# Optimization experiments

Hardware: AMD Instinct MI355X
Metric: run time of the kernel (lower is better)

## Reference

```python
import jax, jax.numpy as jnp
import numpy as np

N_NODES = 50000   # num graph nodes
N_EDGES = 800000  # avg degree 16
D = 96            # in_channels == out_channels (residual aggr_out + x)


def setup_inputs() -> dict:
    key = jax.random.key(0)
    k0, k1, k2, k3, k4 = jax.random.split(key, 5)
    x = jax.random.normal(k0, (N_NODES, D), dtype=jnp.float32)
    edge_index = jax.random.randint(k1, (2, N_EDGES), 0, N_NODES)  # [2,E]: row0=src(j), row1=dst(i)
    edge_weight = jax.random.uniform(k2, (N_EDGES,), dtype=jnp.float32)
    pagerank = jax.random.uniform(k3, (N_NODES,), dtype=jnp.float32)
    # nn.Linear(in_channels, out_channels) params
    W = jax.random.normal(k4, (D, D), dtype=jnp.float32) / np.sqrt(D).astype(np.float32)
    b = jnp.zeros((D,), dtype=jnp.float32)
    return {"x": x, "edge_index": edge_index, "edge_weight": edge_weight,
            "pagerank": pagerank, "W": W, "b": b}


def reference(x, edge_index, edge_weight, pagerank, W, b):
    # CGCConv (PyG MessagePassing, aggr='add', flow source_to_target):
    #   message: edge_weight * x_j * pagerank_j   (gather from source nodes)
    #   aggregate: scatter-add to destination nodes
    #   update: Linear(aggr_out + x)
    src = edge_index[0]
    dst = edge_index[1]
    # [E, D] messages: per-edge gather-multiply
    msgs = edge_weight[:, None] * x[src] * pagerank[src][:, None]
    aggr = jax.ops.segment_sum(msgs, dst, num_segments=x.shape[0])  # [N, D]
    return (aggr + x) @ W.T + b
```

## Files before the change

kernel.cpp:

```cpp
#include <hip/hip_runtime.h>


constexpr int NN = 50000;
constexpr int NE = 800000;
constexpr int DD = 96;
constexpr int NB = 196;
constexpr int CAPB = 4608;
constexpr int EPB = 4096;
constexpr int NBLK = (NE + EPB - 1) / EPB;
constexpr int NCVT = (NN * DD / 4 + 511) / 512;

using s8v = __attribute__((ext_vector_type(8))) short;
using f4v = __attribute__((ext_vector_type(4))) float;

__device__ inline unsigned short f2bf(float f) {
    unsigned u = __float_as_uint(f);
    return (unsigned short)((u + 0x7FFFu + ((u >> 16) & 1u)) >> 16);
}
__device__ inline float bfh(unsigned short v) {
    return __uint_as_float((unsigned)v << 16);
}
__device__ inline unsigned long long pack_e(int meta, float c) {
    return (unsigned long long)(unsigned)meta |
           ((unsigned long long)(unsigned)__float_as_uint(c) << 32);
}

__global__ __launch_bounds__(256) void k_zero(int* __restrict__ cur1) {
    if (threadIdx.x < NB) cur1[threadIdx.x] = 0;
}

__global__ __launch_bounds__(512) void k_prep(const int* __restrict__ src,
                                              const int* __restrict__ dst,
                                              const float* __restrict__ ew,
                                              const float* __restrict__ pr,
                                              int* __restrict__ cur1,
                                              unsigned long long* __restrict__ stage,
                                              const float4* __restrict__ x4,
                                              ushort4* __restrict__ y16v) {
    int tid = threadIdx.x;
    if (blockIdx.x >= NBLK) {
        int i = (blockIdx.x - NBLK) * 512 + tid;
        if (i < NN * DD / 4) {
            float4 v = x4[i];
            y16v[i] = make_ushort4(f2bf(v.x), f2bf(v.y), f2bf(v.z), f2bf(v.w));
        }
        return;
    }
    __shared__ int h[256];
    __shared__ int gb[256];
    __shared__ int sc[256];
    __shared__ unsigned long long sorted[EPB];
    for (int i = tid; i < 256; i += 512) h[i] = 0;
    __syncthreads();
    int base = blockIdx.x * EPB;
    int n = min(EPB, NE - base);

    unsigned long long ent[8]; int bkt[8]; int lrk[8];
    #pragma unroll
    for (int j = 0; j < 8; j++) {
        int e = base + j * 512 + tid;
        bkt[j] = -1;
        if (e < NE) {
            int d = dst[e];
            int s = src[e];
            float c = ew[e] * pr[s];
            int bk = d >> 8;
            bkt[j] = bk;
            lrk[j] = atomicAdd(&h[bk], 1);
            ent[j] = pack_e(s | ((d & 255) << 16) | (bk << 24), c);
        }
    }
    __syncthreads();
    if (tid < 256) sc[tid] = h[tid];
    __syncthreads();
    #pragma unroll
    for (int o = 1; o < 256; o <<= 1) {
        int t = 0;
        if (tid < 256 && tid >= o) t = sc[tid - o];
        __syncthreads();
        if (tid < 256) sc[tid] += t;
        __syncthreads();
    }
    for (int i = tid; i < NB; i += 512)
        gb[i] = h[i] ? atomicAdd(&cur1[i], h[i]) : 0;
    __syncthreads();
    #pragma unroll
    for (int j = 0; j < 8; j++)
        if (bkt[j] >= 0)
            sorted[sc[bkt[j]] - h[bkt[j]] + lrk[j]] = ent[j];
    __syncthreads();
    for (int i = tid; i < n; i += 512) {
        unsigned long long e = sorted[i];
        int bk = ((int)(e >> 24)) & 0xff;
        stage[(size_t)bk * CAPB + gb[bk] + (i - (sc[bk] - h[bk]))] = e;
    }
}

__global__ __launch_bounds__(512) void k_sortB(unsigned long long* __restrict__ stage,
                                               const int* __restrict__ cur1,
                                               int* __restrict__ offs,
                                               int* __restrict__ counts) {
    __shared__ int h[256];
    __shared__ int sc[256];
    __shared__ unsigned sorted[CAPB];
    int b = blockIdx.x;
    int tid = threadIdx.x;
    size_t base = (size_t)b * CAPB;
    int n = cur1[b];

    for (int i = tid; i < 256; i += 512) h[i] = 0;
    __syncthreads();

    unsigned e32[9]; int dl[9]; int lrk[9];
    int m = 0;
    for (int i = tid; i < n; i += 512) {
        unsigned long long e = stage[base + i];
        int dloc = ((int)(e >> 16)) & 0xff;
        unsigned cb = (unsigned)(e >> 32);
        unsigned cbf = (cb + 0x7FFFu + ((cb >> 16) & 1u)) >> 16;
        e32[m] = ((unsigned)e & 0xffffu) | (cbf << 16);
        dl[m] = dloc;
        lrk[m] = atomicAdd(&h[dloc], 1);
        m++;
    }
    __syncthreads();
    if (tid < 256) sc[tid] = h[tid];
    __syncthreads();
    #pragma unroll
    for (int o = 1; o < 256; o <<= 1) {
        int t = 0;
        if (tid < 256 && tid >= o) t = sc[tid - o];
        __syncthreads();
        if (tid < 256) sc[tid] += t;
        __syncthreads();
    }
    m = 0;
    for (int i = tid; i < n; i += 512) {
        sorted[sc[dl[m]] - h[dl[m]] + lrk[m]] = e32[m];
        m++;
    }
    __syncthreads();
    unsigned* outp = (unsigned*)(stage + base);
    for (int i = tid; i < n; i += 512) outp[i] = sorted[i];
    if (tid < 256) {
        int d = (b << 8) + tid;
        if (d < NN) {
            offs[d] = (int)(2 * base) + sc[tid] - h[tid];
            counts[d] = h[tid];
        }
    }
}

__global__ __launch_bounds__(256) void k_pull(const ushort4* __restrict__ y16v,
                                              const float4* __restrict__ x4,
                                              const int* __restrict__ offs,
                                              const int* __restrict__ counts,
                                              const unsigned* __restrict__ ep,
                                              ushort4* __restrict__ io16v) {
    int g = blockIdx.x * 8 + (threadIdx.x >> 5);
    int lane = threadIdx.x & 31;
    if (g >= NN || lane >= 24) return;
    int beg = offs[g];
    int deg = counts[g];
    float ax = 0.f, ay = 0.f, az = 0.f, aw = 0.f;
    int k = 0;
    for (; k + 8 <= deg; k += 8) {
        unsigned e[8];
        #pragma unroll
        for (int j = 0; j < 8; j++) e[j] = ep[beg + k + j];
        ushort4 u[8];
        #pragma unroll
        for (int j = 0; j < 8; j++)
            u[j] = y16v[(size_t)(e[j] & 0xffff) * 24 + lane];
        #pragma unroll
        for (int j = 0; j < 8; j++) {
            float c = bfh((unsigned short)(e[j] >> 16));
            ax += c * bfh(u[j].x);
            ay += c * bfh(u[j].y);
            az += c * bfh(u[j].z);
            aw += c * bfh(u[j].w);
        }
    }
    for (; k + 4 <= deg; k += 4) {
        unsigned e[4];
        #pragma unroll
        for (int j = 0; j < 4; j++) e[j] = ep[beg + k + j];
        ushort4 u[4];
        #pragma unroll
        for (int j = 0; j < 4; j++)
            u[j] = y16v[(size_t)(e[j] & 0xffff) * 24 + lane];
        #pragma unroll
        for (int j = 0; j < 4; j++) {
            float c = bfh((unsigned short)(e[j] >> 16));
            ax += c * bfh(u[j].x);
            ay += c * bfh(u[j].y);
            az += c * bfh(u[j].z);
            aw += c * bfh(u[j].w);
        }
    }
    for (; k < deg; k++) {
        unsigned e = ep[beg + k];
        ushort4 u = y16v[(size_t)(e & 0xffff) * 24 + lane];
        float c = bfh((unsigned short)(e >> 16));
        ax += c * bfh(u.x);
        ay += c * bfh(u.y);
        az += c * bfh(u.z);
        aw += c * bfh(u.w);
    }
    float4 xn = x4[(size_t)g * 24 + lane];
    io16v[(size_t)g * 24 + lane] = make_ushort4(f2bf(ax + xn.x), f2bf(ay + xn.y),
                                                f2bf(az + xn.z), f2bf(aw + xn.w));
}

__global__ __launch_bounds__(256) void k_gemm(const unsigned short* __restrict__ io16,
                                              const float* __restrict__ W,
                                              const float* __restrict__ b,
                                              float* __restrict__ out) {
    __shared__ short bfr[18 * 64 * 8];
    int tid = threadIdx.x;
    for (int i = tid; i < 18 * 512; i += 256) {
        int f = i >> 9, r = i & 511;
        int lane = r >> 3, j = r & 7;
        int ks = f / 6, nt = f - 6 * ks;
        int n = nt * 16 + (lane & 15);
        int k = ks * 32 + (lane >> 4) * 8 + j;
        bfr[i] = (short)f2bf(W[n * DD + k]);
    }
    __syncthreads();

    int wave = tid >> 6, lane = tid & 63;
    int quad = lane >> 4, m16 = lane & 15;
    int r0 = blockIdx.x * 64 + wave * 16;
    int rowa = r0 + m16;
    if (rowa >= NN) rowa = NN - 1;

    f4v acc[6];
    #pragma unroll
    for (int nt = 0; nt < 6; nt++) acc[nt] = (f4v){0.f, 0.f, 0.f, 0.f};

    #pragma unroll
    for (int ks = 0; ks < 3; ks++) {
        s8v a = *(const s8v*)(io16 + (size_t)rowa * DD + ks * 32 + quad * 8);
        #pragma unroll
        for (int nt = 0; nt < 6; nt++) {
            s8v bb = *(const s8v*)&bfr[((ks * 6 + nt) * 64 + lane) * 8];
            acc[nt] = __builtin_amdgcn_mfma_f32_16x16x32_bf16(a, bb, acc[nt], 0, 0, 0);
        }
    }

    #pragma unroll
    for (int nt = 0; nt < 6; nt++) {
        float bias = b[nt * 16 + m16];
        #pragma unroll
        for (int reg = 0; reg < 4; reg++) {
            int rr = r0 + quad * 4 + reg;
            if (rr < NN)
                out[(size_t)rr * DD + nt * 16 + m16] = acc[nt][reg] + bias;
        }
    }
}

extern "C" void kernel_launch(void* const* d_in, const int* in_sizes, int n_in,
                              void* d_out, int out_size, void* d_ws, size_t ws_size,
                              hipStream_t stream) {
    const float* x  = (const float*)d_in[0];
    const int*   ei = (const int*)d_in[1];
    const float* ew = (const float*)d_in[2];
    const float* pr = (const float*)d_in[3];
    const float* W  = (const float*)d_in[4];
    const float* b  = (const float*)d_in[5];
    float* out = (float*)d_out;

    unsigned long long* stage = (unsigned long long*)d_ws;
    unsigned short* y16 = (unsigned short*)(stage + (size_t)NB * CAPB);
    int* cur1   = (int*)(y16 + (size_t)NN * DD);
    int* offs   = cur1 + NB;
    int* counts = offs + NN;
    unsigned short* io16 = (unsigned short*)(counts + NN);

    const int* src = ei;
    const int* dst = ei + NE;

    k_zero<<<1, 256, 0, stream>>>(cur1);
    k_prep<<<NBLK + NCVT, 512, 0, stream>>>(src, dst, ew, pr, cur1, stage,
                                            (const float4*)x, (ushort4*)y16);
    k_sortB<<<NB, 512, 0, stream>>>(stage, cur1, offs, counts);
    k_pull<<<(NN + 7) / 8, 256, 0, stream>>>((const ushort4*)y16, (const float4*)x,
                                             offs, counts, (const unsigned*)stage,
                                             (ushort4*)io16);
    k_gemm<<<(NN + 63) / 64, 256, 0, stream>>>(io16, W, b, out);
}
```

Measured before the change: 141.5 us.

## Pad per-node edge segments to multiples of four for vectorized edge loads

```diff
diff --git a/kernel.cpp b/kernel.cpp
--- a/kernel.cpp
+++ b/kernel.cpp
@@ -101,8 +101,8 @@
                                                int* __restrict__ offs,
                                                int* __restrict__ counts) {
     __shared__ int h[256];
-    __shared__ int sc[256];
-    __shared__ unsigned sorted[CAPB];
+    __shared__ int pc[256];
+    __shared__ unsigned sorted[CAPB + 768];
     int b = blockIdx.x;
     int tid = threadIdx.x;
     size_t base = (size_t)b * CAPB;
@@ -124,28 +124,33 @@
         m++;
     }
     __syncthreads();
-    if (tid < 256) sc[tid] = h[tid];
+    if (tid < 256) pc[tid] = (h[tid] + 3) & ~3;
     __syncthreads();
     #pragma unroll
     for (int o = 1; o < 256; o <<= 1) {
         int t = 0;
-        if (tid < 256 && tid >= o) t = sc[tid - o];
+        if (tid < 256 && tid >= o) t = pc[tid - o];
         __syncthreads();
-        if (tid < 256) sc[tid] += t;
+        if (tid < 256) pc[tid] += t;
         __syncthreads();
     }
+    int ptot = pc[255];
+    for (int i = tid; i < ptot; i += 512) sorted[i] = 0;
+    __syncthreads();
     m = 0;
     for (int i = tid; i < n; i += 512) {
-        sorted[sc[dl[m]] - h[dl[m]] + lrk[m]] = e32[m];
+        int d = dl[m];
+        int pbeg = pc[d] - ((h[d] + 3) & ~3);
+        sorted[pbeg + lrk[m]] = e32[m];
         m++;
     }
     __syncthreads();
     unsigned* outp = (unsigned*)(stage + base);
-    for (int i = tid; i < n; i += 512) outp[i] = sorted[i];
+    for (int i = tid; i < ptot; i += 512) outp[i] = sorted[i];
     if (tid < 256) {
         int d = (b << 8) + tid;
         if (d < NN) {
-            offs[d] = (int)(2 * base) + sc[tid] - h[tid];
+            offs[d] = (int)(2 * base) + pc[tid] - ((h[tid] + 3) & ~3);
             counts[d] = h[tid];
         }
     }
@@ -161,13 +166,31 @@
     int lane = threadIdx.x & 31;
     if (g >= NN || lane >= 24) return;
     int beg = offs[g];
-    int deg = counts[g];
+    int degp = (counts[g] + 3) & ~3;
+    const uint4* ep4 = (const uint4*)(ep + beg);
     float ax = 0.f, ay = 0.f, az = 0.f, aw = 0.f;
     int k = 0;
-    for (; k + 8 <= deg; k += 8) {
-        unsigned e[8];
-        #pragma unroll
-        for (int j = 0; j < 8; j++) e[j] = ep[beg + k + j];
+    for (; k + 16 <= degp; k += 16) {
+        uint4 E0 = ep4[(k >> 2)], E1 = ep4[(k >> 2) + 1];
+        uint4 E2 = ep4[(k >> 2) + 2], E3 = ep4[(k >> 2) + 3];
+        unsigned e[16] = {E0.x, E0.y, E0.z, E0.w, E1.x, E1.y, E1.z, E1.w,
+                          E2.x, E2.y, E2.z, E2.w, E3.x, E3.y, E3.z, E3.w};
+        ushort4 u[16];
+        #pragma unroll
+        for (int j = 0; j < 16; j++)
+            u[j] = y16v[(size_t)(e[j] & 0xffff) * 24 + lane];
+        #pragma unroll
+        for (int j = 0; j < 16; j++) {
+            float c = bfh((unsigned short)(e[j] >> 16));
+            ax += c * bfh(u[j].x);
+            ay += c * bfh(u[j].y);
+            az += c * bfh(u[j].z);
+            aw += c * bfh(u[j].w);
+        }
+    }
+    for (; k + 8 <= degp; k += 8) {
+        uint4 E0 = ep4[(k >> 2)], E1 = ep4[(k >> 2) + 1];
+        unsigned e[8] = {E0.x, E0.y, E0.z, E0.w, E1.x, E1.y, E1.z, E1.w};
         ushort4 u[8];
         #pragma unroll
         for (int j = 0; j < 8; j++)
@@ -181,10 +204,9 @@
             aw += c * bfh(u[j].w);
         }
     }
-    for (; k + 4 <= deg; k += 4) {
-        unsigned e[4];
-        #pragma unroll
-        for (int j = 0; j < 4; j++) e[j] = ep[beg + k + j];
+    for (; k < degp; k += 4) {
+        uint4 E0 = ep4[(k >> 2)];
+        unsigned e[4] = {E0.x, E0.y, E0.z, E0.w};
         ushort4 u[4];
         #pragma unroll
         for (int j = 0; j < 4; j++)
@@ -197,15 +219,6 @@
             az += c * bfh(u[j].z);
             aw += c * bfh(u[j].w);
         }
-    }
-    for (; k < deg; k++) {
-        unsigned e = ep[beg + k];
-        ushort4 u = y16v[(size_t)(e & 0xffff) * 24 + lane];
-        float c = bfh((unsigned short)(e >> 16));
-        ax += c * bfh(u.x);
-        ay += c * bfh(u.y);
-        az += c * bfh(u.z);
-        aw += c * bfh(u.w);
     }
     float4 xn = x4[(size_t)g * 24 + lane];
     io16v[(size_t)g * 24 + lane] = make_ushort4(f2bf(ax + xn.x), f2bf(ay + xn.y),
```

Result: no change. 142.6 us (+0.8%).

## Fuse all stages into one cooperative persistent kernel with grid syncs

Applied to the files above, without the earlier changes.

```diff
diff --git a/kernel.cpp b/kernel.cpp
--- a/kernel.cpp
+++ b/kernel.cpp
@@ -1,4 +1,7 @@
 #include <hip/hip_runtime.h>
+#include <hip/hip_cooperative_groups.h>
+
+namespace cg = cooperative_groups;
 
 
 constexpr int NN = 50000;
@@ -8,7 +11,8 @@
 constexpr int CAPB = 4608;
 constexpr int EPB = 4096;
 constexpr int NBLK = (NE + EPB - 1) / EPB;
-constexpr int NCVT = (NN * DD / 4 + 511) / 512;
+constexpr int NCVT_T = (NN * DD / 4 + 511) / 512;
+constexpr int GRID_MAX = 1024;
 
 using s8v = __attribute__((ext_vector_type(8))) short;
 using f4v = __attribute__((ext_vector_type(4))) float;
@@ -25,237 +29,241 @@
            ((unsigned long long)(unsigned)__float_as_uint(c) << 32);
 }
 
-__global__ __launch_bounds__(256) void k_zero(int* __restrict__ cur1) {
-    if (threadIdx.x < NB) cur1[threadIdx.x] = 0;
-}
-
-__global__ __launch_bounds__(512) void k_prep(const int* __restrict__ src,
-                                              const int* __restrict__ dst,
-                                              const float* __restrict__ ew,
-                                              const float* __restrict__ pr,
-                                              int* __restrict__ cur1,
-                                              unsigned long long* __restrict__ stage,
-                                              const float4* __restrict__ x4,
-                                              ushort4* __restrict__ y16v) {
-    int tid = threadIdx.x;
-    if (blockIdx.x >= NBLK) {
-        int i = (blockIdx.x - NBLK) * 512 + tid;
+__global__ __launch_bounds__(512)
+void k_mega(const int* __restrict__ src, const int* __restrict__ dst,
+            const float* __restrict__ ew, const float* __restrict__ pr,
+            const float4* __restrict__ x4, ushort4* __restrict__ y16v,
+            unsigned long long* __restrict__ stage, int* __restrict__ cur1,
+            int* __restrict__ offs, int* __restrict__ counts,
+            unsigned short* __restrict__ io16,
+            const float* __restrict__ W, const float* __restrict__ bias,
+            float* __restrict__ out) {
+    __shared__ __align__(16) char smem[37120];
+    cg::grid_group grid = cg::this_grid();
+    int tid = threadIdx.x, bid = blockIdx.x, G = gridDim.x;
+
+    if (bid == 0 && tid < NB) cur1[tid] = 0;
+    grid.sync();
+
+    if (bid < NBLK) {
+        unsigned long long* psort = (unsigned long long*)smem;
+        int* h  = (int*)(smem + 32768);
+        int* gb = (int*)(smem + 33792);
+        int* sc = (int*)(smem + 34816);
+        for (int i = tid; i < 256; i += 512) h[i] = 0;
+        __syncthreads();
+        int base = bid * EPB;
+        int n = min(EPB, NE - base);
+
+        unsigned long long ent[8]; int bkt[8]; int lrk[8];
+        #pragma unroll
+        for (int j = 0; j < 8; j++) {
+            int e = base + j * 512 + tid;
+            bkt[j] = -1;
+            if (e < NE) {
+                int d = dst[e];
+                int s = src[e];
+                float c = ew[e] * pr[s];
+                int bk = d >> 8;
+                bkt[j] = bk;
+                lrk[j] = atomicAdd(&h[bk], 1);
+                ent[j] = pack_e(s | ((d & 255) << 16) | (bk << 24), c);
+            }
+        }
+        __syncthreads();
+        if (tid < 256) sc[tid] = h[tid];
+        __syncthreads();
+        #pragma unroll
+        for (int o = 1; o < 256; o <<= 1) {
+            int t = 0;
+            if (tid < 256 && tid >= o) t = sc[tid - o];
+            __syncthreads();
+            if (tid < 256) sc[tid] += t;
+            __syncthreads();
+        }
+        for (int i = tid; i < NB; i += 512)
+            gb[i] = h[i] ? atomicAdd(&cur1[i], h[i]) : 0;
+        __syncthreads();
+        #pragma unroll
+        for (int j = 0; j < 8; j++)
+            if (bkt[j] >= 0)
+                psort[sc[bkt[j]] - h[bkt[j]] + lrk[j]] = ent[j];
+        __syncthreads();
+        for (int i = tid; i < n; i += 512) {
+            unsigned long long e = psort[i];
+            int bk = ((int)(e >> 24)) & 0xff;
+            stage[(size_t)bk * CAPB + gb[bk] + (i - (sc[bk] - h[bk]))] = e;
+        }
+    }
+    for (int t = bid; t < NCVT_T; t += G) {
+        int i = t * 512 + tid;
         if (i < NN * DD / 4) {
             float4 v = x4[i];
             y16v[i] = make_ushort4(f2bf(v.x), f2bf(v.y), f2bf(v.z), f2bf(v.w));
         }
-        return;
-    }
-    __shared__ int h[256];
-    __shared__ int gb[256];
-    __shared__ int sc[256];
-    __shared__ unsigned long long sorted[EPB];
-    for (int i = tid; i < 256; i += 512) h[i] = 0;
-    __syncthreads();
-    int base = blockIdx.x * EPB;
-    int n = min(EPB, NE - base);
-
-    unsigned long long ent[8]; int bkt[8]; int lrk[8];
-    #pragma unroll
-    for (int j = 0; j < 8; j++) {
-        int e = base + j * 512 + tid;
-        bkt[j] = -1;
-        if (e < NE) {
-            int d = dst[e];
-            int s = src[e];
-            float c = ew[e] * pr[s];
-            int bk = d >> 8;
-            bkt[j] = bk;
-            lrk[j] = atomicAdd(&h[bk], 1);
-            ent[j] = pack_e(s | ((d & 255) << 16) | (bk << 24), c);
-        }
-    }
-    __syncthreads();
-    if (tid < 256) sc[tid] = h[tid];
-    __syncthreads();
-    #pragma unroll
-    for (int o = 1; o < 256; o <<= 1) {
-        int t = 0;
-        if (tid < 256 && tid >= o) t = sc[tid - o];
-        __syncthreads();
-        if (tid < 256) sc[tid] += t;
-        __syncthreads();
-    }
-    for (int i = tid; i < NB; i += 512)
-        gb[i] = h[i] ? atomicAdd(&cur1[i], h[i]) : 0;
-    __syncthreads();
-    #pragma unroll
-    for (int j = 0; j < 8; j++)
-        if (bkt[j] >= 0)
-            sorted[sc[bkt[j]] - h[bkt[j]] + lrk[j]] = ent[j];
-    __syncthreads();
-    for (int i = tid; i < n; i += 512) {
-        unsigned long long e = sorted[i];
-        int bk = ((int)(e >> 24)) & 0xff;
-        stage[(size_t)bk * CAPB + gb[bk] + (i - (sc[bk] - h[bk]))] = e;
-    }
-}
-
-__global__ __launch_bounds__(512) void k_sortB(unsigned long long* __restrict__ stage,
-                                               const int* __restrict__ cur1,
-                                               int* __restrict__ offs,
-                                               int* __restrict__ counts) {
-    __shared__ int h[256];
-    __shared__ int sc[256];
-    __shared__ unsigned sorted[CAPB];
-    int b = blockIdx.x;
-    int tid = threadIdx.x;
-    size_t base = (size_t)b * CAPB;
-    int n = cur1[b];
-
-    for (int i = tid; i < 256; i += 512) h[i] = 0;
-    __syncthreads();
-
-    unsigned e32[9]; int dl[9]; int lrk[9];
-    int m = 0;
-    for (int i = tid; i < n; i += 512) {
-        unsigned long long e = stage[base + i];
-        int dloc = ((int)(e >> 16)) & 0xff;
-        unsigned cb = (unsigned)(e >> 32);
-        unsigned cbf = (cb + 0x7FFFu + ((cb >> 16) & 1u)) >> 16;
-        e32[m] = ((unsigned)e & 0xffffu) | (cbf << 16);
-        dl[m] = dloc;
-        lrk[m] = atomicAdd(&h[dloc], 1);
-        m++;
-    }
-    __syncthreads();
-    if (tid < 256) sc[tid] = h[tid];
-    __syncthreads();
-    #pragma unroll
-    for (int o = 1; o < 256; o <<= 1) {
-        int t = 0;
-        if (tid < 256 && tid >= o) t = sc[tid - o];
-        __syncthreads();
-        if (tid < 256) sc[tid] += t;
-        __syncthreads();
-    }
-    m = 0;
-    for (int i = tid; i < n; i += 512) {
-        sorted[sc[dl[m]] - h[dl[m]] + lrk[m]] = e32[m];
-        m++;
-    }
-    __syncthreads();
-    unsigned* outp = (unsigned*)(stage + base);
-    for (int i = tid; i < n; i += 512) outp[i] = sorted[i];
-    if (tid < 256) {
-        int d = (b << 8) + tid;
-        if (d < NN) {
-            offs[d] = (int)(2 * base) + sc[tid] - h[tid];
-            counts[d] = h[tid];
-        }
-    }
-}
-
-__global__ __launch_bounds__(256) void k_pull(const ushort4* __restrict__ y16v,
-                                              const float4* __restrict__ x4,
-                                              const int* __restrict__ offs,
-                                              const int* __restrict__ counts,
-                                              const unsigned* __restrict__ ep,
-                                              ushort4* __restrict__ io16v) {
-    int g = blockIdx.x * 8 + (threadIdx.x >> 5);
-    int lane = threadIdx.x & 31;
-    if (g >= NN || lane >= 24) return;
-    int beg = offs[g];
-    int deg = counts[g];
-    float ax = 0.f, ay = 0.f, az = 0.f, aw = 0.f;
-    int k = 0;
-    for (; k + 8 <= deg; k += 8) {
-        unsigned e[8];
+    }
+    grid.sync();
+
+    for (int b = bid; b < NB; b += G) {
+        unsigned* ssort = (unsigned*)smem;
+        int* h  = (int*)(smem + 18432);
+        int* sc = (int*)(smem + 19456);
+        size_t base = (size_t)b * CAPB;
+        int n = cur1[b];
+
+        for (int i = tid; i < 256; i += 512) h[i] = 0;
+        __syncthreads();
+
+        unsigned e32[9]; int dl[9]; int lrk[9];
+        int m = 0;
+        for (int i = tid; i < n; i += 512) {
+            unsigned long long e = stage[base + i];
+            int dloc = ((int)(e >> 16)) & 0xff;
+            unsigned cb = (unsigned)(e >> 32);
+            unsigned cbf = (cb + 0x7FFFu + ((cb >> 16) & 1u)) >> 16;
+            e32[m] = ((unsigned)e & 0xffffu) | (cbf << 16);
+            dl[m] = dloc;
+            lrk[m] = atomicAdd(&h[dloc], 1);
+            m++;
+        }
+        __syncthreads();
+        if (tid < 256) sc[tid] = h[tid];
+        __syncthreads();
         #pragma unroll
-        for (int j = 0; j < 8; j++) e[j] = ep[beg + k + j];
-        ushort4 u[8];
-        #pragma unroll
-        for (int j = 0; j < 8; j++)
-            u[j] = y16v[(size_t)(e[j] & 0xffff) * 24 + lane];
-        #pragma unroll
-        for (int j = 0; j < 8; j++) {
-            float c = bfh((unsigned short)(e[j] >> 16));
-            ax += c * bfh(u[j].x);
-            ay += c * bfh(u[j].y);
-            az += c * bfh(u[j].z);
-            aw += c * bfh(u[j].w);
-        }
-    }
-    for (; k + 4 <= deg; k += 4) {
-        unsigned e[4];
-        #pragma unroll
-        for (int j = 0; j < 4; j++) e[j] = ep[beg + k + j];
-        ushort4 u[4];
-        #pragma unroll
-        for (int j = 0; j < 4; j++)
-            u[j] = y16v[(size_t)(e[j] & 0xffff) * 24 + lane];
-        #pragma unroll
-        for (int j = 0; j < 4; j++) {
-            float c = bfh((unsigned short)(e[j] >> 16));
-            ax += c * bfh(u[j].x);
-            ay += c * bfh(u[j].y);
-            az += c * bfh(u[j].z);
-            aw += c * bfh(u[j].w);
-        }
-    }
-    for (; k < deg; k++) {
-        unsigned e = ep[beg + k];
-        ushort4 u = y16v[(size_t)(e & 0xffff) * 24 + lane];
-        float c = bfh((unsigned short)(e >> 16));
-        ax += c * bfh(u.x);
-        ay += c * bfh(u.y);
-        az += c * bfh(u.z);
-        aw += c * bfh(u.w);
-    }
-    float4 xn = x4[(size_t)g * 24 + lane];
-    io16v[(size_t)g * 24 + lane] = make_ushort4(f2bf(ax + xn.x), f2bf(ay + xn.y),
-                                                f2bf(az + xn.z), f2bf(aw + xn.w));
-}
-
-__global__ __launch_bounds__(256) void k_gemm(const unsigned short* __restrict__ io16,
-                                              const float* __restrict__ W,
-                                              const float* __restrict__ b,
-                                              float* __restrict__ out) {
-    __shared__ short bfr[18 * 64 * 8];
-    int tid = threadIdx.x;
-    for (int i = tid; i < 18 * 512; i += 256) {
-        int f = i >> 9, r = i & 511;
-        int lane = r >> 3, j = r & 7;
-        int ks = f / 6, nt = f - 6 * ks;
-        int n = nt * 16 + (lane & 15);
-        int k = ks * 32 + (lane >> 4) * 8 + j;
-        bfr[i] = (short)f2bf(W[n * DD + k]);
-    }
-    __syncthreads();
-
-    int wave = tid >> 6, lane = tid & 63;
-    int quad = lane >> 4, m16 = lane & 15;
-    int r0 = blockIdx.x * 64 + wave * 16;
-    int rowa = r0 + m16;
-    if (rowa >= NN) rowa = NN - 1;
-
-    f4v acc[6];
-    #pragma unroll
-    for (int nt = 0; nt < 6; nt++) acc[nt] = (f4v){0.f, 0.f, 0.f, 0.f};
-
-    #pragma unroll
-    for (int ks = 0; ks < 3; ks++) {
-        s8v a = *(const s8v*)(io16 + (size_t)rowa * DD + ks * 32 + quad * 8);
-        #pragma unroll
-        for (int nt = 0; nt < 6; nt++) {
-            s8v bb = *(const s8v*)&bfr[((ks * 6 + nt) * 64 + lane) * 8];
-            acc[nt] = __builtin_amdgcn_mfma_f32_16x16x32_bf16(a, bb, acc[nt], 0, 0, 0);
-        }
-    }
-
-    #pragma unroll
-    for (int nt = 0; nt < 6; nt++) {
-        float bias = b[nt * 16 + m16];
-        #pragma unroll
-        for (int reg = 0; reg < 4; reg++) {
-            int rr = r0 + quad * 4 + reg;
-            if (rr < NN)
-                out[(size_t)rr * DD + nt * 16 + m16] = acc[nt][reg] + bias;
+        for (int o = 1; o < 256; o <<= 1) {
+            int t = 0;
+            if (tid < 256 && tid >= o) t = sc[tid - o];
+            __syncthreads();
+            if (tid < 256) sc[tid] += t;
+            __syncthreads();
+        }
+        m = 0;
+        for (int i = tid; i < n; i += 512) {
+            ssort[sc[dl[m]] - h[dl[m]] + lrk[m]] = e32[m];
+            m++;
+        }
+        __syncthreads();
+        unsigned* outp = (unsigned*)(stage + base);
+        for (int i = tid; i < n; i += 512) outp[i] = ssort[i];
+        if (tid < 256) {
+            int d = (b << 8) + tid;
+            if (d < NN) {
+                offs[d] = (int)(2 * base) + sc[tid] - h[tid];
+                counts[d] = h[tid];
+            }
+        }
+        __syncthreads();
+    }
+    grid.sync();
+
+    {
+        const ushort4* yv = (const ushort4*)y16v;
+        const unsigned* ep = (const unsigned*)stage;
+        ushort4* iov = (ushort4*)io16;
+        int ngrp = (NN + 15) / 16;
+        int sub = tid >> 5, lane = tid & 31;
+        for (int gi = bid; gi < ngrp; gi += G) {
+            int g = gi * 16 + sub;
+            if (g >= NN || lane >= 24) continue;
+            int beg = offs[g];
+            int deg = counts[g];
+            float ax = 0.f, ay = 0.f, az = 0.f, aw = 0.f;
+            int k = 0;
+            for (; k + 8 <= deg; k += 8) {
+                unsigned e[8];
+                #pragma unroll
+                for (int j = 0; j < 8; j++) e[j] = ep[beg + k + j];
+                ushort4 u[8];
+                #pragma unroll
+                for (int j = 0; j < 8; j++)
+                    u[j] = yv[(size_t)(e[j] & 0xffff) * 24 + lane];
+                #pragma unroll
+                for (int j = 0; j < 8; j++) {
+                    float c = bfh((unsigned short)(e[j] >> 16));
+                    ax += c * bfh(u[j].x);
+                    ay += c * bfh(u[j].y);
+                    az += c * bfh(u[j].z);
+                    aw += c * bfh(u[j].w);
+                }
+            }
+            for (; k + 4 <= deg; k += 4) {
+                unsigned e[4];
+                #pragma unroll
+                for (int j = 0; j < 4; j++) e[j] = ep[beg + k + j];
+                ushort4 u[4];
+                #pragma unroll
+                for (int j = 0; j < 4; j++)
+                    u[j] = yv[(size_t)(e[j] & 0xffff) * 24 + lane];
+                #pragma unroll
+                for (int j = 0; j < 4; j++) {
+                    float c = bfh((unsigned short)(e[j] >> 16));
+                    ax += c * bfh(u[j].x);
+                    ay += c * bfh(u[j].y);
+                    az += c * bfh(u[j].z);
+                    aw += c * bfh(u[j].w);
+                }
+            }
+            for (; k < deg; k++) {
+                unsigned e = ep[beg + k];
+                ushort4 u = yv[(size_t)(e & 0xffff) * 24 + lane];
+                float c = bfh((unsigned short)(e >> 16));
+                ax += c * bfh(u.x);
+                ay += c * bfh(u.y);
+                az += c * bfh(u.z);
+                aw += c * bfh(u.w);
+            }
+            float4 xn = x4[(size_t)g * 24 + lane];
+            iov[(size_t)g * 24 + lane] = make_ushort4(
+                f2bf(ax + xn.x), f2bf(ay + xn.y), f2bf(az + xn.z), f2bf(aw + xn.w));
+        }
+    }
+    grid.sync();
+
+    {
+        short* bfr = (short*)smem;
+        for (int i = tid; i < 18 * 512; i += 512) {
+            int f = i >> 9, r = i & 511;
+            int lane = r >> 3, j = r & 7;
+            int ks = f / 6, nt = f - 6 * ks;
+            int n = nt * 16 + (lane & 15);
+            int k = ks * 32 + (lane >> 4) * 8 + j;
+            bfr[i] = (short)f2bf(W[n * DD + k]);
+        }
+        __syncthreads();
+
+        int wave = tid >> 6, lane = tid & 63;
+        int quad = lane >> 4, m16 = lane & 15;
+        int niter = (NN + 127) / 128;
+        for (int it = bid; it < niter; it += G) {
+            int r0 = it * 128 + wave * 16;
+            int rowa = r0 + m16;
+            if (rowa >= NN) rowa = NN - 1;
+
+            f4v acc[6];
+            #pragma unroll
+            for (int nt = 0; nt < 6; nt++) acc[nt] = (f4v){0.f, 0.f, 0.f, 0.f};
+
+            #pragma unroll
+            for (int ks = 0; ks < 3; ks++) {
+                s8v a = *(const s8v*)(io16 + (size_t)rowa * DD + ks * 32 + quad * 8);
+                #pragma unroll
+                for (int nt = 0; nt < 6; nt++) {
+                    s8v bb = *(const s8v*)&bfr[((ks * 6 + nt) * 64 + lane) * 8];
+                    acc[nt] = __builtin_amdgcn_mfma_f32_16x16x32_bf16(a, bb, acc[nt],
+                                                                      0, 0, 0);
+                }
+            }
+
+            #pragma unroll
+            for (int nt = 0; nt < 6; nt++) {
+                float bv = bias[nt * 16 + m16];
+                #pragma unroll
+                for (int reg = 0; reg < 4; reg++) {
+                    int rr = r0 + quad * 4 + reg;
+                    if (rr < NN)
+                        out[(size_t)rr * DD + nt * 16 + m16] = acc[nt][reg] + bv;
+                }
+            }
         }
     }
 }
@@ -280,13 +288,19 @@
 
     const int* src = ei;
     const int* dst = ei + NE;
-
-    k_zero<<<1, 256, 0, stream>>>(cur1);
-    k_prep<<<NBLK + NCVT, 512, 0, stream>>>(src, dst, ew, pr, cur1, stage,
-                                            (const float4*)x, (ushort4*)y16);
-    k_sortB<<<NB, 512, 0, stream>>>(stage, cur1, offs, counts);
-    k_pull<<<(NN + 7) / 8, 256, 0, stream>>>((const ushort4*)y16, (const float4*)x,
-                                             offs, counts, (const unsigned*)stage,
-                                             (ushort4*)io16);
-    k_gemm<<<(NN + 63) / 64, 256, 0, stream>>>(io16, W, b, out);
-}
+    const float4* x4 = (const float4*)x;
+    ushort4* y16v = (ushort4*)y16;
+
+    int nb = 0;
+    hipOccupancyMaxActiveBlocksPerMultiprocessor(&nb, (const void*)k_mega, 512, 0);
+    if (nb < 1) nb = 1;
+    long grid = (long)nb * 256;
+    if (grid > GRID_MAX) grid = GRID_MAX;
+
+    void* args[] = {(void*)&src, (void*)&dst, (void*)&ew, (void*)&pr,
+                    (void*)&x4, (void*)&y16v, (void*)&stage, (void*)&cur1,
+                    (void*)&offs, (void*)&counts, (void*)&io16,
+                    (void*)&W, (void*)&b, (void*)&out};
+    hipLaunchCooperativeKernel((const void*)k_mega, dim3((unsigned)grid), dim3(512),
+                               args, 0, stream);
+}
```

After: 284.7 us. 2.01x slower.

## Fuse gather-aggregate with bf16 MFMA GEMM via shared-memory tile

Applied to the files above, without the earlier changes.

```diff
diff --git a/kernel.cpp b/kernel.cpp
--- a/kernel.cpp
+++ b/kernel.cpp
@@ -8,7 +8,8 @@
 constexpr int CAPB = 4608;
 constexpr int EPB = 4096;
 constexpr int NBLK = (NE + EPB - 1) / EPB;
-constexpr int NCVT = (NN * DD / 4 + 511) / 512;
+constexpr int NCVT_T = (NN * DD / 4 + 511) / 512;
+constexpr int XS = 104;
 
 using s8v = __attribute__((ext_vector_type(8))) short;
 using f4v = __attribute__((ext_vector_type(4))) float;
@@ -23,10 +24,6 @@
 __device__ inline unsigned long long pack_e(int meta, float c) {
     return (unsigned long long)(unsigned)meta |
            ((unsigned long long)(unsigned)__float_as_uint(c) << 32);
-}
-
-__global__ __launch_bounds__(256) void k_zero(int* __restrict__ cur1) {
-    if (threadIdx.x < NB) cur1[threadIdx.x] = 0;
 }
 
 __global__ __launch_bounds__(512) void k_prep(const int* __restrict__ src,
@@ -36,13 +33,27 @@
                                               int* __restrict__ cur1,
                                               unsigned long long* __restrict__ stage,
                                               const float4* __restrict__ x4,
-                                              ushort4* __restrict__ y16v) {
+                                              ushort4* __restrict__ y16v,
+                                              const float* __restrict__ W,
+                                              unsigned short* __restrict__ wfrag) {
     int tid = threadIdx.x;
     if (blockIdx.x >= NBLK) {
-        int i = (blockIdx.x - NBLK) * 512 + tid;
-        if (i < NN * DD / 4) {
-            float4 v = x4[i];
-            y16v[i] = make_ushort4(f2bf(v.x), f2bf(v.y), f2bf(v.z), f2bf(v.w));
+        int t = blockIdx.x - NBLK;
+        if (t < NCVT_T) {
+            int i = t * 512 + tid;
+            if (i < NN * DD / 4) {
+                float4 v = x4[i];
+                y16v[i] = make_ushort4(f2bf(v.x), f2bf(v.y), f2bf(v.z), f2bf(v.w));
+            }
+        } else {
+            for (int i = tid; i < 18 * 512; i += 512) {
+                int f = i >> 9, r = i & 511;
+                int lane = r >> 3, j = r & 7;
+                int ks = f / 6, nt = f - 6 * ks;
+                int n = nt * 16 + (lane & 15);
+                int k = ks * 32 + (lane >> 4) * 8 + j;
+                wfrag[i] = f2bf(W[n * DD + k]);
+            }
         }
         return;
     }
@@ -151,88 +162,81 @@
     }
 }
 
-__global__ __launch_bounds__(256) void k_pull(const ushort4* __restrict__ y16v,
-                                              const float4* __restrict__ x4,
-                                              const int* __restrict__ offs,
-                                              const int* __restrict__ counts,
-                                              const unsigned* __restrict__ ep,
-                                              ushort4* __restrict__ io16v) {
-    int g = blockIdx.x * 8 + (threadIdx.x >> 5);
-    int lane = threadIdx.x & 31;
-    if (g >= NN || lane >= 24) return;
-    int beg = offs[g];
-    int deg = counts[g];
-    float ax = 0.f, ay = 0.f, az = 0.f, aw = 0.f;
-    int k = 0;
-    for (; k + 8 <= deg; k += 8) {
-        unsigned e[8];
-        #pragma unroll
-        for (int j = 0; j < 8; j++) e[j] = ep[beg + k + j];
-        ushort4 u[8];
-        #pragma unroll
-        for (int j = 0; j < 8; j++)
-            u[j] = y16v[(size_t)(e[j] & 0xffff) * 24 + lane];
-        #pragma unroll
-        for (int j = 0; j < 8; j++) {
-            float c = bfh((unsigned short)(e[j] >> 16));
-            ax += c * bfh(u[j].x);
-            ay += c * bfh(u[j].y);
-            az += c * bfh(u[j].z);
-            aw += c * bfh(u[j].w);
-        }
-    }
-    for (; k + 4 <= deg; k += 4) {
-        unsigned e[4];
-        #pragma unroll
-        for (int j = 0; j < 4; j++) e[j] = ep[beg + k + j];
-        ushort4 u[4];
-        #pragma unroll
-        for (int j = 0; j < 4; j++)
-            u[j] = y16v[(size_t)(e[j] & 0xffff) * 24 + lane];
-        #pragma unroll
-        for (int j = 0; j < 4; j++) {
-            float c = bfh((unsigned short)(e[j] >> 16));
-            ax += c * bfh(u[j].x);
-            ay += c * bfh(u[j].y);
-            az += c * bfh(u[j].z);
-            aw += c * bfh(u[j].w);
-        }
-    }
-    for (; k < deg; k++) {
-        unsigned e = ep[beg + k];
-        ushort4 u = y16v[(size_t)(e & 0xffff) * 24 + lane];
-        float c = bfh((unsigned short)(e >> 16));
-        ax += c * bfh(u.x);
-        ay += c * bfh(u.y);
-        az += c * bfh(u.z);
-        aw += c * bfh(u.w);
-    }
-    float4 xn = x4[(size_t)g * 24 + lane];
-    io16v[(size_t)g * 24 + lane] = make_ushort4(f2bf(ax + xn.x), f2bf(ay + xn.y),
-                                                f2bf(az + xn.z), f2bf(aw + xn.w));
-}
-
-__global__ __launch_bounds__(256) void k_gemm(const unsigned short* __restrict__ io16,
-                                              const float* __restrict__ W,
-                                              const float* __restrict__ b,
-                                              float* __restrict__ out) {
-    __shared__ short bfr[18 * 64 * 8];
+__global__ __launch_bounds__(256) void k_pullgemm(const ushort4* __restrict__ y16v,
+                                                  const float4* __restrict__ x4,
+                                                  const int* __restrict__ offs,
+                                                  const int* __restrict__ counts,
+                                                  const unsigned* __restrict__ ep,
+                                                  const unsigned short* __restrict__ wfrag,
+                                                  const float* __restrict__ bias,
+                                                  float* __restrict__ out) {
+    __shared__ unsigned short xt[64 * XS];
     int tid = threadIdx.x;
-    for (int i = tid; i < 18 * 512; i += 256) {
-        int f = i >> 9, r = i & 511;
-        int lane = r >> 3, j = r & 7;
-        int ks = f / 6, nt = f - 6 * ks;
-        int n = nt * 16 + (lane & 15);
-        int k = ks * 32 + (lane >> 4) * 8 + j;
-        bfr[i] = (short)f2bf(W[n * DD + k]);
-    }
-    __syncthreads();
-
-    int wave = tid >> 6, lane = tid & 63;
-    int quad = lane >> 4, m16 = lane & 15;
-    int r0 = blockIdx.x * 64 + wave * 16;
-    int rowa = r0 + m16;
-    if (rowa >= NN) rowa = NN - 1;
+    int sub = tid >> 5, lane = tid & 31;
+    int gbase = blockIdx.x * 64;
+
+    #pragma unroll
+    for (int i = 0; i < 8; i++) {
+        int lr = sub * 8 + i;
+        int g = gbase + lr;
+        if (g < NN && lane < 24) {
+            int beg = offs[g];
+            int deg = counts[g];
+            float ax = 0.f, ay = 0.f, az = 0.f, aw = 0.f;
+            int k = 0;
+            for (; k + 8 <= deg; k += 8) {
+                unsigned e[8];
+                #pragma unroll
+                for (int j = 0; j < 8; j++) e[j] = ep[beg + k + j];
+                ushort4 u[8];
+                #pragma unroll
+                for (int j = 0; j < 8; j++)
+                    u[j] = y16v[(size_t)(e[j] & 0xffff) * 24 + lane];
+                #pragma unroll
+                for (int j = 0; j < 8; j++) {
+                    float c = bfh((unsigned short)(e[j] >> 16));
+                    ax += c * bfh(u[j].x);
+                    ay += c * bfh(u[j].y);
+                    az += c * bfh(u[j].z);
+                    aw += c * bfh(u[j].w);
+                }
+            }
+            for (; k + 4 <= deg; k += 4) {
+                unsigned e[4];
+                #pragma unroll
+                for (int j = 0; j < 4; j++) e[j] = ep[beg + k + j];
+                ushort4 u[4];
+                #pragma unroll
+                for (int j = 0; j < 4; j++)
+                    u[j] = y16v[(size_t)(e[j] & 0xffff) * 24 + lane];
+                #pragma unroll
+                for (int j = 0; j < 4; j++) {
+                    float c = bfh((unsigned short)(e[j] >> 16));
+                    ax += c * bfh(u[j].x);
+                    ay += c * bfh(u[j].y);
+                    az += c * bfh(u[j].z);
+                    aw += c * bfh(u[j].w);
+                }
+            }
+            for (; k < deg; k++) {
+                unsigned e = ep[beg + k];
+                ushort4 u = y16v[(size_t)(e & 0xffff) * 24 + lane];
+                float c = bfh((unsigned short)(e >> 16));
+                ax += c * bfh(u.x);
+                ay += c * bfh(u.y);
+                az += c * bfh(u.z);
+                aw += c * bfh(u.w);
+            }
+            float4 xn = x4[(size_t)g * 24 + lane];
+            *(ushort4*)&xt[lr * XS + lane * 4] = make_ushort4(
+                f2bf(ax + xn.x), f2bf(ay + xn.y), f2bf(az + xn.z), f2bf(aw + xn.w));
+        }
+    }
+    __syncthreads();
+
+    int wave = tid >> 6, l64 = tid & 63;
+    int quad = l64 >> 4, m16 = l64 & 15;
+    int r0 = wave * 16;
 
     f4v acc[6];
     #pragma unroll
@@ -240,22 +244,22 @@
 
     #pragma unroll
     for (int ks = 0; ks < 3; ks++) {
-        s8v a = *(const s8v*)(io16 + (size_t)rowa * DD + ks * 32 + quad * 8);
+        s8v a = *(const s8v*)&xt[(r0 + m16) * XS + ks * 32 + quad * 8];
         #pragma unroll
         for (int nt = 0; nt < 6; nt++) {
-            s8v bb = *(const s8v*)&bfr[((ks * 6 + nt) * 64 + lane) * 8];
+            s8v bb = *(const s8v*)&wfrag[((ks * 6 + nt) * 64 + l64) * 8];
             acc[nt] = __builtin_amdgcn_mfma_f32_16x16x32_bf16(a, bb, acc[nt], 0, 0, 0);
         }
     }
 
     #pragma unroll
     for (int nt = 0; nt < 6; nt++) {
-        float bias = b[nt * 16 + m16];
+        float bv = bias[nt * 16 + m16];
         #pragma unroll
         for (int reg = 0; reg < 4; reg++) {
-            int rr = r0 + quad * 4 + reg;
+            int rr = gbase + r0 + quad * 4 + reg;
             if (rr < NN)
-                out[(size_t)rr * DD + nt * 16 + m16] = acc[nt][reg] + bias;
+                out[(size_t)rr * DD + nt * 16 + m16] = acc[nt][reg] + bv;
         }
     }
 }
@@ -276,17 +280,18 @@
     int* cur1   = (int*)(y16 + (size_t)NN * DD);
     int* offs   = cur1 + NB;
     int* counts = offs + NN;
-    unsigned short* io16 = (unsigned short*)(counts + NN);
+    unsigned short* wfrag = (unsigned short*)(counts + NN);
 
     const int* src = ei;
     const int* dst = ei + NE;
 
-    k_zero<<<1, 256, 0, stream>>>(cur1);
-    k_prep<<<NBLK + NCVT, 512, 0, stream>>>(src, dst, ew, pr, cur1, stage,
-                                            (const float4*)x, (ushort4*)y16);
+    hipMemsetAsync(cur1, 0, NB * sizeof(int), stream);
+    k_prep<<<NBLK + NCVT_T + 1, 512, 0, stream>>>(src, dst, ew, pr, cur1, stage,
+                                                  (const float4*)x, (ushort4*)y16,
+                                                  W, wfrag);
     k_sortB<<<NB, 512, 0, stream>>>(stage, cur1, offs, counts);
-    k_pull<<<(NN + 7) / 8, 256, 0, stream>>>((const ushort4*)y16, (const float4*)x,
-                                             offs, counts, (const unsigned*)stage,
-                                             (ushort4*)io16);
-    k_gemm<<<(NN + 63) / 64, 256, 0, stream>>>(io16, W, b, out);
-}
+    k_pullgemm<<<(NN + 63) / 64, 256, 0, stream>>>((const ushort4*)y16,
+                                                   (const float4*)x, offs, counts,
+                                                   (const unsigned*)stage, wfrag,
+                                                   b, out);
+}
```

After: 148.9 us. 1.05x slower.
